# Kernel optimization log

Hardware: AMD Instinct MI355X
Metric: run time of the kernel (lower is better)

Reference implementation:

```python
import jax, jax.numpy as jnp
import numpy as np

N, C = 16384, 512

def setup_inputs() -> dict:
    key = jax.random.key(0)
    k1, k2 = jax.random.split(key)
    mean = jax.random.normal(k1, (N, C), dtype=jnp.float32)
    var = jax.random.uniform(k2, (N, C), dtype=jnp.float32)  # positive diagonal variances
    return {"mean": mean, "var": var, "num_samples": 400}

def reference(mean, var, num_samples):
    # Monte Carlo estimate of E[softmax(mean + eps)], eps ~ N(0, diag(var)).
    # lax.scan keeps memory flat (no [S, N, C] buffer), matching the torch loop.
    std = jnp.sqrt(var)
    keys = jax.random.split(jax.random.key(42), num_samples)

    def body(acc, k):
        eps = jax.random.normal(k, mean.shape, dtype=mean.dtype) * std
        return acc + jax.nn.softmax(mean + eps, axis=-1), None

    acc, _ = jax.lax.scan(body, jnp.zeros_like(mean), keys)
    return acc / num_samples
```

## Files before the change

kernel.cpp:

```cpp
#include <hip/hip_runtime.h>
#include <stdint.h>

#define NSAMP 400
#define NC 512

#if __has_builtin(__builtin_amdgcn_exp2f)
#define EXP2F(x) __builtin_amdgcn_exp2f(x)
#else
#define EXP2F(x) __expf((x) * 0.6931471805599453f)
#endif
#if __has_builtin(__builtin_amdgcn_logf)
#define LOG2F(x) __builtin_amdgcn_logf(x)
#else
#define LOG2F(x) (__logf(x) * 1.4426950408889634f)
#endif

static __device__ __forceinline__ uint32_t rotl32(uint32_t v, int n) {
  return __builtin_amdgcn_alignbit(v, v, 32u - (uint32_t)n);
}
static __device__ __forceinline__ uint32_t rotl32_s(uint32_t v, int n) {
  return (v << n) | (v >> (32 - n));
}

#define TF_ROUND(x0, x1, R, ROT) \
  x0 += x1; x1 = ROT(x1, R); x1 ^= x0;

static __device__ __forceinline__ void threefry2x32_s(
    uint32_t k0, uint32_t k1, uint32_t x0, uint32_t x1,
    uint32_t& o0, uint32_t& o1)
{
  const uint32_t ks2 = k0 ^ k1 ^ 0x1BD11BDAu;
  x0 += k0; x1 += k1;
  TF_ROUND(x0,x1,13,rotl32_s) TF_ROUND(x0,x1,15,rotl32_s)
  TF_ROUND(x0,x1,26,rotl32_s) TF_ROUND(x0,x1, 6,rotl32_s)
  x0 += k1; x1 += ks2 + 1u;
  TF_ROUND(x0,x1,17,rotl32_s) TF_ROUND(x0,x1,29,rotl32_s)
  TF_ROUND(x0,x1,16,rotl32_s) TF_ROUND(x0,x1,24,rotl32_s)
  x0 += ks2; x1 += k0 + 2u;
  TF_ROUND(x0,x1,13,rotl32_s) TF_ROUND(x0,x1,15,rotl32_s)
  TF_ROUND(x0,x1,26,rotl32_s) TF_ROUND(x0,x1, 6,rotl32_s)
  x0 += k0; x1 += k1 + 3u;
  TF_ROUND(x0,x1,17,rotl32_s) TF_ROUND(x0,x1,29,rotl32_s)
  TF_ROUND(x0,x1,16,rotl32_s) TF_ROUND(x0,x1,24,rotl32_s)
  x0 += k1; x1 += ks2 + 4u;
  TF_ROUND(x0,x1,13,rotl32_s) TF_ROUND(x0,x1,15,rotl32_s)
  TF_ROUND(x0,x1,26,rotl32_s) TF_ROUND(x0,x1, 6,rotl32_s)
  x0 += ks2; x1 += k0 + 5u;
  o0 = x0; o1 = x1;
}

static __device__ __forceinline__ uint32_t tf_bits(
    uint32_t k0, uint32_t k1, uint32_t ks2, uint32_t cnt)
{
  uint32_t x0 = k0;
  uint32_t x1 = cnt + k1;
  TF_ROUND(x0,x1,13,rotl32) TF_ROUND(x0,x1,15,rotl32)
  TF_ROUND(x0,x1,26,rotl32) TF_ROUND(x0,x1, 6,rotl32)
  x0 += k1; x1 += ks2 + 1u;
  TF_ROUND(x0,x1,17,rotl32) TF_ROUND(x0,x1,29,rotl32)
  TF_ROUND(x0,x1,16,rotl32) TF_ROUND(x0,x1,24,rotl32)
  x0 += ks2; x1 += k0 + 2u;
  TF_ROUND(x0,x1,13,rotl32) TF_ROUND(x0,x1,15,rotl32)
  TF_ROUND(x0,x1,26,rotl32) TF_ROUND(x0,x1, 6,rotl32)
  x0 += k0; x1 += k1 + 3u;
  TF_ROUND(x0,x1,17,rotl32) TF_ROUND(x0,x1,29,rotl32)
  TF_ROUND(x0,x1,16,rotl32) TF_ROUND(x0,x1,24,rotl32)
  x0 += k1; x1 += ks2 + 4u;
  TF_ROUND(x0,x1,13,rotl32) TF_ROUND(x0,x1,15,rotl32)
  TF_ROUND(x0,x1,26,rotl32) TF_ROUND(x0,x1, 6,rotl32)
  x0 += ks2; x1 += k0 + 5u;
  return x0 ^ x1;
}

static __device__ __forceinline__ float softexp(float u, float L, float sd2, float m2) {
  float p;
  if (L > -7.2134752f) {
    float w = fmaf(L, -0.69314718f, -2.5f);
    p =              2.81022636e-08f;
    p = fmaf(p, w,   3.43273939e-07f);
    p = fmaf(p, w,  -3.5233877e-06f);
    p = fmaf(p, w,  -4.39150654e-06f);
    p = fmaf(p, w,   0.00021858087f);
    p = fmaf(p, w,  -0.00125372503f);
    p = fmaf(p, w,  -0.00417768164f);
    p = fmaf(p, w,   0.246640727f);
    p = fmaf(p, w,   1.50140941f);
  } else {
    float w = __builtin_amdgcn_sqrtf(L * -0.69314718f) - 3.0f;
    p =             -0.000200214257f;
    p = fmaf(p, w,   0.000100950558f);
    p = fmaf(p, w,   0.00134934322f);
    p = fmaf(p, w,  -0.00367342844f);
    p = fmaf(p, w,   0.00573950773f);
    p = fmaf(p, w,  -0.0076224613f);
    p = fmaf(p, w,   0.00943887047f);
    p = fmaf(p, w,   1.00167406f);
    p = fmaf(p, w,   2.83297682f);
  }
  float px = p * u;
  return EXP2F(fmaf(px, sd2, m2));
}

__global__ __launch_bounds__(256)
void mc_softmax_kernel(const float* __restrict__ mean,
                       const float* __restrict__ var,
                       float* __restrict__ out)
{
  const int lane  = threadIdx.x & 63;
  const int row   = (blockIdx.x << 2) + (threadIdx.x >> 6);
  const int cbase = lane << 2;

  const float* mr = mean + (size_t)row * NC;
  const float* vr = var  + (size_t)row * NC;

  float m2[8], sd2[8], acc[8];
  {
    const float L2E = 1.4426950408889634f;
    const float S2L = 2.0402788959f;
    float4 t0 = *(const float4*)(mr + cbase);
    float4 t1 = *(const float4*)(mr + 256 + cbase);
    m2[0] = t0.x * L2E; m2[1] = t0.y * L2E; m2[2] = t0.z * L2E; m2[3] = t0.w * L2E;
    m2[4] = t1.x * L2E; m2[5] = t1.y * L2E; m2[6] = t1.z * L2E; m2[7] = t1.w * L2E;
    float4 v0 = *(const float4*)(vr + cbase);
    float4 v1 = *(const float4*)(vr + 256 + cbase);
    sd2[0] = __builtin_amdgcn_sqrtf(v0.x) * S2L;
    sd2[1] = __builtin_amdgcn_sqrtf(v0.y) * S2L;
    sd2[2] = __builtin_amdgcn_sqrtf(v0.z) * S2L;
    sd2[3] = __builtin_amdgcn_sqrtf(v0.w) * S2L;
    sd2[4] = __builtin_amdgcn_sqrtf(v1.x) * S2L;
    sd2[5] = __builtin_amdgcn_sqrtf(v1.y) * S2L;
    sd2[6] = __builtin_amdgcn_sqrtf(v1.z) * S2L;
    sd2[7] = __builtin_amdgcn_sqrtf(v1.w) * S2L;
  }
#pragma unroll
  for (int j = 0; j < 8; ++j) acc[j] = 0.0f;

  const uint32_t base = (uint32_t)(row * NC + cbase);
  const float lo = -0.99999994f;

  for (int s = 0; s < NSAMP; ++s) {
    uint32_t k0, k1;
    threefry2x32_s(0u, 42u, 0u, (uint32_t)s, k0, k1);
    const uint32_t ks2 = k0 ^ k1 ^ 0x1BD11BDAu;

    float u8[8], L8[8];
#pragma unroll
    for (int j = 0; j < 8; ++j) {
      const uint32_t cnt = base + (uint32_t)(j < 4 ? j : 252 + j);
      uint32_t bits = tf_bits(k0, k1, ks2, cnt);
      float f = __uint_as_float(__builtin_amdgcn_alignbit(0x7Fu, bits, 9u)) - 1.0f;
      float u = fmaf(f, 2.0f, lo);
      u8[j] = u;
      L8[j] = LOG2F(fmaf(u, -u, 1.0f));
    }

    float e8[8], sum = 0.0f;
#pragma unroll
    for (int j = 0; j < 8; ++j) {
      e8[j] = softexp(u8[j], L8[j], sd2[j], m2[j]);
      sum += e8[j];
    }

#pragma unroll
    for (int off = 32; off >= 1; off >>= 1)
      sum += __shfl_xor(sum, off);
    const float inv = __builtin_amdgcn_rcpf(sum);
#pragma unroll
    for (int j = 0; j < 8; ++j)
      acc[j] = fmaf(e8[j], inv, acc[j]);
  }

  float* orow = out + (size_t)row * NC;
  const float sc = 1.0f / (float)NSAMP;
  float4 o0, o1;
  o0.x = acc[0] * sc; o0.y = acc[1] * sc; o0.z = acc[2] * sc; o0.w = acc[3] * sc;
  o1.x = acc[4] * sc; o1.y = acc[5] * sc; o1.z = acc[6] * sc; o1.w = acc[7] * sc;
  *(float4*)(orow + cbase)       = o0;
  *(float4*)(orow + 256 + cbase) = o1;
}

extern "C" void kernel_launch(void* const* d_in, const int* in_sizes, int n_in,
                              void* d_out, int out_size, void* d_ws, size_t ws_size,
                              hipStream_t stream) {
  const float* mean = (const float*)d_in[0];
  const float* var  = (const float*)d_in[1];
  float* out        = (float*)d_out;

  const int rows = out_size / NC;
  const int blocks = rows / 4;
  mc_softmax_kernel<<<blocks, 256, 0, stream>>>(mean, var, out);
}
```

Baseline: 7.257 ms.

## Precompute per-sample Threefry keys in LDS and fuse key-injection adds

Result: faster. 6.504 ms (-10.4%).

```diff
diff --git a/kernel.cpp b/kernel.cpp
--- a/kernel.cpp
+++ b/kernel.cpp
@@ -16,59 +16,46 @@
 #endif
 
 static __device__ __forceinline__ uint32_t rotl32(uint32_t v, int n) {
-  return __builtin_amdgcn_alignbit(v, v, 32u - (uint32_t)n);
-}
-static __device__ __forceinline__ uint32_t rotl32_s(uint32_t v, int n) {
   return (v << n) | (v >> (32 - n));
 }
 
-#define TF_ROUND(x0, x1, R, ROT) \
-  x0 += x1; x1 = ROT(x1, R); x1 ^= x0;
-
-static __device__ __forceinline__ void threefry2x32_s(
+#define TFS(x0, x1, R) { x0 += x1; x1 = rotl32(x1, R); x1 ^= x0; }
+static __device__ __forceinline__ void threefry2x32_full(
     uint32_t k0, uint32_t k1, uint32_t x0, uint32_t x1,
     uint32_t& o0, uint32_t& o1)
 {
   const uint32_t ks2 = k0 ^ k1 ^ 0x1BD11BDAu;
   x0 += k0; x1 += k1;
-  TF_ROUND(x0,x1,13,rotl32_s) TF_ROUND(x0,x1,15,rotl32_s)
-  TF_ROUND(x0,x1,26,rotl32_s) TF_ROUND(x0,x1, 6,rotl32_s)
+  TFS(x0,x1,13) TFS(x0,x1,15) TFS(x0,x1,26) TFS(x0,x1, 6)
   x0 += k1; x1 += ks2 + 1u;
-  TF_ROUND(x0,x1,17,rotl32_s) TF_ROUND(x0,x1,29,rotl32_s)
-  TF_ROUND(x0,x1,16,rotl32_s) TF_ROUND(x0,x1,24,rotl32_s)
+  TFS(x0,x1,17) TFS(x0,x1,29) TFS(x0,x1,16) TFS(x0,x1,24)
   x0 += ks2; x1 += k0 + 2u;
-  TF_ROUND(x0,x1,13,rotl32_s) TF_ROUND(x0,x1,15,rotl32_s)
-  TF_ROUND(x0,x1,26,rotl32_s) TF_ROUND(x0,x1, 6,rotl32_s)
+  TFS(x0,x1,13) TFS(x0,x1,15) TFS(x0,x1,26) TFS(x0,x1, 6)
   x0 += k0; x1 += k1 + 3u;
-  TF_ROUND(x0,x1,17,rotl32_s) TF_ROUND(x0,x1,29,rotl32_s)
-  TF_ROUND(x0,x1,16,rotl32_s) TF_ROUND(x0,x1,24,rotl32_s)
+  TFS(x0,x1,17) TFS(x0,x1,29) TFS(x0,x1,16) TFS(x0,x1,24)
   x0 += k1; x1 += ks2 + 4u;
-  TF_ROUND(x0,x1,13,rotl32_s) TF_ROUND(x0,x1,15,rotl32_s)
-  TF_ROUND(x0,x1,26,rotl32_s) TF_ROUND(x0,x1, 6,rotl32_s)
+  TFS(x0,x1,13) TFS(x0,x1,15) TFS(x0,x1,26) TFS(x0,x1, 6)
   x0 += ks2; x1 += k0 + 5u;
   o0 = x0; o1 = x1;
 }
 
-static __device__ __forceinline__ uint32_t tf_bits(
-    uint32_t k0, uint32_t k1, uint32_t ks2, uint32_t cnt)
+#define R3OP(R)          { x0 += x1; x1 = rotl32(x1, R) ^ x0; }
+#define INJR(ka, kb, R)  { x1 += kb; x0 = x0 + x1 + ka; x1 = rotl32(x1, R) ^ x0; }
+
+static __device__ __forceinline__ uint32_t tf_bits_fused(
+    uint32_t k0, uint32_t k1, uint32_t ks2,
+    uint32_t I1, uint32_t I2, uint32_t I3, uint32_t I4, uint32_t I5,
+    uint32_t cnt)
 {
-  uint32_t x0 = k0;
   uint32_t x1 = cnt + k1;
-  TF_ROUND(x0,x1,13,rotl32) TF_ROUND(x0,x1,15,rotl32)
-  TF_ROUND(x0,x1,26,rotl32) TF_ROUND(x0,x1, 6,rotl32)
-  x0 += k1; x1 += ks2 + 1u;
-  TF_ROUND(x0,x1,17,rotl32) TF_ROUND(x0,x1,29,rotl32)
-  TF_ROUND(x0,x1,16,rotl32) TF_ROUND(x0,x1,24,rotl32)
-  x0 += ks2; x1 += k0 + 2u;
-  TF_ROUND(x0,x1,13,rotl32) TF_ROUND(x0,x1,15,rotl32)
-  TF_ROUND(x0,x1,26,rotl32) TF_ROUND(x0,x1, 6,rotl32)
-  x0 += k0; x1 += k1 + 3u;
-  TF_ROUND(x0,x1,17,rotl32) TF_ROUND(x0,x1,29,rotl32)
-  TF_ROUND(x0,x1,16,rotl32) TF_ROUND(x0,x1,24,rotl32)
-  x0 += k1; x1 += ks2 + 4u;
-  TF_ROUND(x0,x1,13,rotl32) TF_ROUND(x0,x1,15,rotl32)
-  TF_ROUND(x0,x1,26,rotl32) TF_ROUND(x0,x1, 6,rotl32)
-  x0 += ks2; x1 += k0 + 5u;
+  uint32_t x0 = x1 + k0;
+  x1 = rotl32(x1, 13) ^ x0;
+  R3OP(15) R3OP(26) R3OP(6)
+  INJR(k1,  I1, 17) R3OP(29) R3OP(16) R3OP(24)
+  INJR(ks2, I2, 13) R3OP(15) R3OP(26) R3OP(6)
+  INJR(k0,  I3, 17) R3OP(29) R3OP(16) R3OP(24)
+  INJR(k1,  I4, 13) R3OP(15) R3OP(26) R3OP(6)
+  x0 += ks2; x1 += I5;
   return x0 ^ x1;
 }
 
@@ -106,6 +93,18 @@
                        const float* __restrict__ var,
                        float* __restrict__ out)
 {
+  __shared__ __align__(16) uint32_t kc[NSAMP][8];
+  for (int s = threadIdx.x; s < NSAMP; s += 256) {
+    uint32_t a, b;
+    threefry2x32_full(0u, 42u, 0u, (uint32_t)s, a, b);
+    uint32_t ks2 = a ^ b ^ 0x1BD11BDAu;
+    kc[s][0] = a;        kc[s][1] = b;
+    kc[s][2] = ks2;      kc[s][3] = ks2 + 1u;
+    kc[s][4] = a + 2u;   kc[s][5] = b + 3u;
+    kc[s][6] = ks2 + 4u; kc[s][7] = a + 5u;
+  }
+  __syncthreads();
+
   const int lane  = threadIdx.x & 63;
   const int row   = (blockIdx.x << 2) + (threadIdx.x >> 6);
   const int cbase = lane << 2;
@@ -139,15 +138,16 @@
   const float lo = -0.99999994f;
 
   for (int s = 0; s < NSAMP; ++s) {
-    uint32_t k0, k1;
-    threefry2x32_s(0u, 42u, 0u, (uint32_t)s, k0, k1);
-    const uint32_t ks2 = k0 ^ k1 ^ 0x1BD11BDAu;
+    const uint4 ca = *(const uint4*)&kc[s][0];
+    const uint4 cb = *(const uint4*)&kc[s][4];
+    const uint32_t k0 = ca.x, k1 = ca.y, ks2 = ca.z, I1 = ca.w;
+    const uint32_t I2 = cb.x, I3 = cb.y, I4 = cb.z, I5 = cb.w;
 
     float u8[8], L8[8];
 #pragma unroll
     for (int j = 0; j < 8; ++j) {
       const uint32_t cnt = base + (uint32_t)(j < 4 ? j : 252 + j);
-      uint32_t bits = tf_bits(k0, k1, ks2, cnt);
+      uint32_t bits = tf_bits_fused(k0, k1, ks2, I1, I2, I3, I4, I5, cnt);
       float f = __uint_as_float(__builtin_amdgcn_alignbit(0x7Fu, bits, 9u)) - 1.0f;
       float u = fmaf(f, 2.0f, lo);
       u8[j] = u;
```
